# Kernel optimization log

Measured on AMD Instinct MI355X. Metric: run time of the kernel, lower is better.

Reference implementation:

```python
import jax, jax.numpy as jnp
import numpy as np

B, T, I, H = 512, 256, 64, 512
HN = 30  # hidden_nodes
EPS = 1e-5


def setup_inputs() -> dict:
    key = jax.random.key(0)
    ks = jax.random.split(key, 14)
    s = 0.05
    return {
        "x": jax.random.normal(ks[0], (B, T, I), jnp.float32),
        "W_ih": jax.random.normal(ks[1], (4 * H, I), jnp.float32) * s,
        "W_hh": jax.random.normal(ks[2], (4 * H, H), jnp.float32) * s,
        "b_ih": jax.random.normal(ks[3], (4 * H,), jnp.float32) * s,
        "b_hh": jax.random.normal(ks[4], (4 * H,), jnp.float32) * s,
        "l1_w": jax.random.normal(ks[5], (HN, H), jnp.float32) * s,
        "l1_b": jax.random.normal(ks[6], (HN,), jnp.float32) * s,
        "l2_w": jax.random.normal(ks[7], (HN, HN), jnp.float32) * s,
        "l3_w": jax.random.normal(ks[8], (HN, HN), jnp.float32) * s,
        "l4_w": jax.random.normal(ks[9], (HN, HN), jnp.float32) * s,
        "l5_w": jax.random.normal(ks[10], (2, HN), jnp.float32) * s,
        "bn_gamma": jnp.ones((HN,), jnp.float32),
        "bn_beta": jnp.zeros((HN,), jnp.float32),
    }


def _bn(a, gamma, beta):
    # training-mode BatchNorm1d: batch statistics over axis 0 (biased var)
    m = jnp.mean(a, axis=0)
    v = jnp.mean((a - m) ** 2, axis=0)
    return gamma * (a - m) * jax.lax.rsqrt(v + EPS) + beta


def reference(x, W_ih, W_hh, b_ih, b_hh, l1_w, l1_b, l2_w, l3_w, l4_w, l5_w,
              bn_gamma, bn_beta):
    def mlp(h):
        a = _bn(h @ l1_w.T + l1_b, bn_gamma, bn_beta)
        a = jax.nn.relu(a)
        a = jax.nn.relu(_bn(a @ l2_w.T, bn_gamma, bn_beta))
        a = jax.nn.relu(_bn(a @ l3_w.T, bn_gamma, bn_beta))
        a = jax.nn.relu(_bn(a @ l4_w.T, bn_gamma, bn_beta))
        return a @ l5_w.T  # [B, 2]

    def step(carry, x_t):
        h, c = carry
        gates = x_t @ W_ih.T + b_ih + h @ W_hh.T + b_hh  # [B, 4H]
        i_g, f_g, g_g, o_g = jnp.split(gates, 4, axis=1)  # torch order: i,f,g,o
        c = jax.nn.sigmoid(f_g) * c + jax.nn.sigmoid(i_g) * jnp.tanh(g_g)
        h = jax.nn.sigmoid(o_g) * jnp.tanh(c)
        return (h, c), mlp(h)

    h0 = jnp.zeros((x.shape[0], H), x.dtype)
    c0 = jnp.zeros((x.shape[0], H), x.dtype)
    xs = jnp.swapaxes(x, 0, 1)  # [T, B, I]
    _, outs = jax.lax.scan(step, (h0, c0), xs)  # [T, B, 2]
    return jnp.transpose(outs, (1, 2, 0))  # [B, 2, T]
```

## Files before the change

### kernel.cpp

```cpp
#include <hip/hip_runtime.h>
#include <math.h>

#define B_  512
#define T_  256
#define I_  64
#define H_  512
#define G4  2048
#define K_  576
#define HN  30
#define EPSf 1e-5f
#define GW  8
#define NG  32
#define BM  16
#define BJ  64
#define KP  520
#define A1P 32
#define HROT 4

typedef __attribute__((ext_vector_type(8))) short short8;
typedef __attribute__((ext_vector_type(4))) float f32x4;

static __device__ __forceinline__ unsigned short f2bf(float f) {
    unsigned int u = __float_as_uint(f);
    u += 0x7fffu + ((u >> 16) & 1u);
    return (unsigned short)(u >> 16);
}
static __device__ __forceinline__ float sigf(float x) {
    return __builtin_amdgcn_rcpf(1.0f + __expf(-x));
}
static __device__ __forceinline__ float tanh_f(float x) {
    float e = __expf(-2.0f * fabsf(x));
    float r = (1.0f - e) * __builtin_amdgcn_rcpf(1.0f + e);
    return copysignf(r, x);
}

__global__ void pack_kernel(const float* __restrict__ x, const float* __restrict__ Wih,
                            const float* __restrict__ Whh, const float* __restrict__ bih,
                            const float* __restrict__ bhh, const float* __restrict__ l1w,
                            unsigned short* __restrict__ Wp, unsigned short* __restrict__ xb,
                            float* __restrict__ bias, unsigned short* __restrict__ hb,
                            float* __restrict__ a1p, unsigned short* __restrict__ wl1b,
                            unsigned int* __restrict__ arr, unsigned int* __restrict__ map) {
    const int stride = gridDim.x * blockDim.x;
    const int g0 = blockIdx.x * blockDim.x + threadIdx.x;
    for (int idx = g0; idx < G4 * K_; idx += stride) {
        int n = idx / K_, k = idx - n * K_;
        float v = (k < H_) ? Whh[n * H_ + k] : Wih[n * I_ + (k - H_)];
        Wp[idx] = f2bf(v);
    }
    for (int idx = g0; idx < T_ * B_ * I_; idx += stride) {
        int t = idx / (B_ * I_);
        int r = idx - t * (B_ * I_);
        int b = r / I_, i = r - b * I_;
        xb[idx] = f2bf(x[((size_t)b * T_ + t) * I_ + i]);
    }
    for (int idx = g0; idx < G4; idx += stride) bias[idx] = bih[idx] + bhh[idx];
    for (int idx = g0; idx < B_ * H_; idx += stride) hb[idx] = 0;
    for (int idx = g0; idx < T_ * B_ * A1P; idx += stride) a1p[idx] = 0.0f;
    for (int idx = g0; idx < 32 * H_; idx += stride) {
        int f = idx >> 9, k = idx & 511;
        wl1b[idx] = (f < HN) ? f2bf(l1w[f * H_ + k]) : 0;
    }
    for (int idx = g0; idx < NG * 64; idx += stride) arr[idx] = 0u;
    for (int idx = g0; idx < 256; idx += stride) map[idx] = 0u;
}

__global__ __launch_bounds__(256, 1) void lstm_kernel(
        const unsigned short* __restrict__ Wp, const unsigned short* __restrict__ xb,
        const float* __restrict__ bias, unsigned short* __restrict__ hb,
        float* __restrict__ a1p, const unsigned short* __restrict__ wl1b,
        unsigned int* __restrict__ arr, unsigned int* __restrict__ map) {
    __shared__ unsigned short As[BM][KP];
    __shared__ unsigned short hsb[BM][72];
    __shared__ int flagLDS;

    const int tid  = threadIdx.x;
    const int w    = tid >> 6;
    const int lane = tid & 63;
    const int r    = lane & 15;
    const int q    = lane >> 4;
    const int mb   = blockIdx.x & 31;
    const int jb   = blockIdx.x >> 5;
    const int m0   = mb * BM;
    const int j0   = jb * BJ;
    const int hrow = tid >> 4, hseg = tid & 15;
    const int ft_l1 = w >> 1, kt_l1 = w & 1;

    if (tid == 0) {
        unsigned xcc;
        asm volatile("s_getreg_b32 %0, hwreg(HW_REG_XCC_ID)" : "=s"(xcc));
        __hip_atomic_store(&map[blockIdx.x], 0x100u | (xcc & 0xffu),
                           __ATOMIC_RELAXED, __HIP_MEMORY_SCOPE_AGENT);
    }

    short8 bfrag[4][18];
#pragma unroll
    for (int g = 0; g < 4; ++g)
#pragma unroll
        for (int kc = 0; kc < 18; ++kc) {
            bfrag[g][kc] = *reinterpret_cast<const short8*>(
                Wp + (size_t)(g * H_ + j0 + w * 16 + r) * K_ + kc * 32 + q * 8);
            asm volatile("" : "+v"(bfrag[g][kc]));
        }
    short8 bl1 = *reinterpret_cast<const short8*>(
        wl1b + (size_t)(ft_l1 * 16 + r) * H_ + j0 + kt_l1 * 32 + q * 8);
    asm volatile("" : "+v"(bl1));

    float bias_g[4];
#pragma unroll
    for (int g = 0; g < 4; ++g) bias_g[g] = bias[g * H_ + j0 + w * 16 + r];

    float c[4] = {0.f, 0.f, 0.f, 0.f};
    unsigned int* ctrA = arr + mb * 64;
    unsigned int* ctrB = arr + mb * 64 + 32;
    int fastf = 0;

#pragma unroll 1
    for (int t = 0; t < T_; ++t) {
        const unsigned short* hin = hb + (size_t)(t % HROT) * B_ * H_;
        unsigned short* hout      = hb + (size_t)((t + 1) % HROT) * B_ * H_;

        if (t > 0) {
            if (tid == 0) {
                if (fastf) {
                    const unsigned target = (unsigned)(GW * (t - 1));
                    unsigned tries = 0;
                    for (;;) {
                        unsigned old, zero = 0;
                        asm volatile("global_atomic_add %0, %1, %2, off sc0\n\t"
                                     "s_waitcnt vmcnt(0)"
                                     : "=&v"(old) : "v"(ctrB), "v"(zero) : "memory");
                        if (old >= target) break;
                        if (++tries > 100000u) break;
                        __builtin_amdgcn_s_sleep(1);
                    }
                } else {
                    const unsigned target = (unsigned)(GW * t);
                    unsigned tries = 0;
                    while (__hip_atomic_load(ctrA, __ATOMIC_RELAXED,
                                             __HIP_MEMORY_SCOPE_AGENT) < target) {
                        if (++tries > 100000u) break;
                        __builtin_amdgcn_s_sleep(1);
                    }
                    if (t == 1) {
                        unsigned v0 = __hip_atomic_load(&map[mb], __ATOMIC_RELAXED,
                                                        __HIP_MEMORY_SCOPE_AGENT);
                        int same = (v0 & 0x100u) ? 1 : 0;
                        for (int u = 1; u < GW; ++u) {
                            unsigned vu = __hip_atomic_load(&map[u * 32 + mb],
                                                            __ATOMIC_RELAXED,
                                                            __HIP_MEMORY_SCOPE_AGENT);
                            same &= (vu == v0);
                        }
                        flagLDS = same;
                    }
                }
            }
            __syncthreads();
            if (t == 1) fastf = flagLDS;
            asm volatile("" ::: "memory");
        }

        const unsigned short* xr = xb + ((size_t)t * B_ + m0 + r) * I_ + q * 8;
        const short8 xf0 = *reinterpret_cast<const short8*>(xr);
        const short8 xf1 = *reinterpret_cast<const short8*>(xr + 32);

        short8 hv[4];
        const unsigned short* hbase = hin + (size_t)(m0 + hrow) * H_ + hseg * 8;
        if (fastf) {
#pragma unroll
            for (int u = 0; u < 4; ++u)
                asm volatile("global_load_dwordx4 %0, %1, off sc0"
                             : "=&v"(hv[u]) : "v"(hbase + u * 128));
        } else {
#pragma unroll
            for (int u = 0; u < 4; ++u) {
                unsigned long long p2[2];
                p2[0] = __hip_atomic_load((const unsigned long long*)(hbase + u * 128),
                                          __ATOMIC_RELAXED, __HIP_MEMORY_SCOPE_AGENT);
                p2[1] = __hip_atomic_load((const unsigned long long*)(hbase + u * 128 + 4),
                                          __ATOMIC_RELAXED, __HIP_MEMORY_SCOPE_AGENT);
                __builtin_memcpy(&hv[u], p2, 16);
            }
        }
        asm volatile("s_waitcnt vmcnt(0)" ::: "memory");
        __builtin_amdgcn_sched_barrier(0);
#pragma unroll
        for (int u = 0; u < 4; ++u)
            *reinterpret_cast<short8*>(&As[hrow][u * 128 + hseg * 8]) = hv[u];
        __syncthreads();

        f32x4 acc[4];
#pragma unroll
        for (int g = 0; g < 4; ++g)
            acc[g] = (f32x4){bias_g[g], bias_g[g], bias_g[g], bias_g[g]};
#pragma unroll
        for (int kc = 0; kc < 16; ++kc) {
            const short8 afr = *reinterpret_cast<const short8*>(
                &As[r][kc * 32 + q * 8]);
#pragma unroll
            for (int g = 0; g < 4; ++g)
                acc[g] = __builtin_amdgcn_mfma_f32_16x16x32_bf16(
                    afr, bfrag[g][kc], acc[g], 0, 0, 0);
        }
#pragma unroll
        for (int g = 0; g < 4; ++g) {
            acc[g] = __builtin_amdgcn_mfma_f32_16x16x32_bf16(xf0, bfrag[g][16], acc[g], 0, 0, 0);
            acc[g] = __builtin_amdgcn_mfma_f32_16x16x32_bf16(xf1, bfrag[g][17], acc[g], 0, 0, 0);
        }

#pragma unroll
        for (int rr = 0; rr < 4; ++rr) {
            float ig = acc[0][rr], fg = acc[1][rr], gg = acc[2][rr], og = acc[3][rr];
            float cn = sigf(fg) * c[rr] + sigf(ig) * tanh_f(gg);
            c[rr] = cn;
            hsb[q * 4 + rr][w * 16 + r] = f2bf(sigf(og) * tanh_f(cn));
        }
        __syncthreads();

        {
            unsigned long long pv;
            __builtin_memcpy(&pv, &hsb[hrow][hseg * 4], 8);
            unsigned long long* hdst = (unsigned long long*)(hout
                + (size_t)(m0 + hrow) * H_ + j0 + hseg * 4);
            if (fastf) *hdst = pv;
            else __hip_atomic_store(hdst, pv, __ATOMIC_RELAXED,
                                    __HIP_MEMORY_SCOPE_AGENT);
        }

        if (t + 1 < T_) {
            asm volatile("s_waitcnt vmcnt(0)" ::: "memory");
            __syncthreads();
            if (tid == 0) {
                if (fastf) {
                    unsigned one = 1;
                    asm volatile("global_atomic_add %0, %1, off"
                                 :: "v"(ctrB), "v"(one) : "memory");
                } else {
                    __hip_atomic_fetch_add(ctrA, 1u, __ATOMIC_RELAXED,
                                           __HIP_MEMORY_SCOPE_AGENT);
                }
            }
        } else {
            __syncthreads();
        }

        const short8 ah = *reinterpret_cast<const short8*>(
            &hsb[r][kt_l1 * 32 + q * 8]);
        f32x4 d = __builtin_amdgcn_mfma_f32_16x16x32_bf16(
            ah, bl1, (f32x4){0.f, 0.f, 0.f, 0.f}, 0, 0, 0);
        const int f = ft_l1 * 16 + r;
        if (f < HN) {
            float* dst = a1p + ((size_t)t * B_ + m0 + q * 4) * A1P + f;
            if (fastf) {
#pragma unroll
                for (int rr = 0; rr < 4; ++rr) {
                    float* p = dst + rr * A1P;
                    asm volatile("global_atomic_add_f32 %0, %1, off"
                                 :: "v"(p), "v"(d[rr]) : "memory");
                }
            } else {
#pragma unroll
                for (int rr = 0; rr < 4; ++rr)
                    __hip_atomic_fetch_add(dst + rr * A1P, d[rr], __ATOMIC_RELAXED,
                                           __HIP_MEMORY_SCOPE_AGENT);
            }
        }
    }
}

static __device__ __forceinline__ void bn_relu30(float v[HN], const float* __restrict__ gamma,
                                                 const float* __restrict__ beta,
                                                 float (*pS)[HN], float (*pQ)[HN]) {
    float s0[HN], s1[HN];
#pragma unroll
    for (int f = 0; f < HN; ++f) { s0[f] = v[f]; s1[f] = v[f] * v[f]; }
#pragma unroll
    for (int off = 32; off >= 1; off >>= 1) {
#pragma unroll
        for (int f = 0; f < HN; ++f) {
            s0[f] += __shfl_xor(s0[f], off);
            s1[f] += __shfl_xor(s1[f], off);
        }
    }
    const int lane = threadIdx.x & 63, w = threadIdx.x >> 6;
    if (lane == 0) {
#pragma unroll
        for (int f = 0; f < HN; ++f) { pS[w][f] = s0[f]; pQ[w][f] = s1[f]; }
    }
    __syncthreads();
#pragma unroll
    for (int f = 0; f < HN; ++f) {
        float S = 0.f, Q = 0.f;
#pragma unroll
        for (int u = 0; u < 8; ++u) { S += pS[u][f]; Q += pQ[u][f]; }
        float m = S * (1.0f / 512.0f);
        float var = Q * (1.0f / 512.0f) - m * m;
        float inv = 1.0f / sqrtf(var + EPSf);
        float tv = gamma[f] * (v[f] - m) * inv + beta[f];
        v[f] = fmaxf(tv, 0.f);
    }
    __syncthreads();
}

static __device__ __forceinline__ void layer30(float v[HN], const float* __restrict__ w) {
    float u[HN];
#pragma unroll
    for (int f = 0; f < HN; ++f) {
        float a = 0.f;
#pragma unroll
        for (int k = 0; k < HN; ++k) a = fmaf(v[k], w[f * HN + k], a);
        u[f] = a;
    }
#pragma unroll
    for (int f = 0; f < HN; ++f) v[f] = u[f];
}

__global__ __launch_bounds__(512) void mlp_kernel(
        const float* __restrict__ a1p, const float* __restrict__ l1b,
        const float* __restrict__ l2w, const float* __restrict__ l3w,
        const float* __restrict__ l4w, const float* __restrict__ l5w,
        const float* __restrict__ gamma, const float* __restrict__ beta,
        float* __restrict__ out) {
    const int t = blockIdx.x;
    const int b = threadIdx.x;
    __shared__ float pS[8][HN], pQ[8][HN];
    float v[HN];
    const float* src = a1p + ((size_t)t * B_ + b) * A1P;
#pragma unroll
    for (int f = 0; f < HN; ++f) v[f] = src[f] + l1b[f];
    bn_relu30(v, gamma, beta, pS, pQ);
    layer30(v, l2w); bn_relu30(v, gamma, beta, pS, pQ);
    layer30(v, l3w); bn_relu30(v, gamma, beta, pS, pQ);
    layer30(v, l4w); bn_relu30(v, gamma, beta, pS, pQ);
    float o0 = 0.f, o1 = 0.f;
#pragma unroll
    for (int k = 0; k < HN; ++k) {
        o0 = fmaf(v[k], l5w[k], o0);
        o1 = fmaf(v[k], l5w[HN + k], o1);
    }
    out[(size_t)b * (2 * T_) + t]      = o0;
    out[(size_t)b * (2 * T_) + T_ + t] = o1;
}

extern "C" void kernel_launch(void* const* d_in, const int* in_sizes, int n_in,
                              void* d_out, int out_size, void* d_ws, size_t ws_size,
                              hipStream_t stream) {
    const float* x    = (const float*)d_in[0];
    const float* Wih  = (const float*)d_in[1];
    const float* Whh  = (const float*)d_in[2];
    const float* bih  = (const float*)d_in[3];
    const float* bhh  = (const float*)d_in[4];
    const float* l1w  = (const float*)d_in[5];
    const float* l1b  = (const float*)d_in[6];
    const float* l2w  = (const float*)d_in[7];
    const float* l3w  = (const float*)d_in[8];
    const float* l4w  = (const float*)d_in[9];
    const float* l5w  = (const float*)d_in[10];
    const float* gam  = (const float*)d_in[11];
    const float* bet  = (const float*)d_in[12];
    float* out = (float*)d_out;

    char* ws = (char*)d_ws;
    unsigned short* Wp   = (unsigned short*)ws;  ws += (size_t)G4 * K_ * 2;
    unsigned short* xb   = (unsigned short*)ws;  ws += (size_t)T_ * B_ * I_ * 2;
    float*          bia  = (float*)ws;           ws += (size_t)G4 * 4;
    unsigned short* hb   = (unsigned short*)ws;  ws += (size_t)HROT * B_ * H_ * 2;
    float*          a1p  = (float*)ws;           ws += (size_t)T_ * B_ * A1P * 4;
    unsigned short* wl1b = (unsigned short*)ws;  ws += (size_t)32 * H_ * 2;
    unsigned int*   arr  = (unsigned int*)ws;    ws += (size_t)NG * 64 * 4;
    unsigned int*   map  = (unsigned int*)ws;    ws += (size_t)256 * 4;

    pack_kernel<<<1024, 256, 0, stream>>>(x, Wih, Whh, bih, bhh, l1w,
                                          Wp, xb, bia, hb, a1p, wl1b, arr, map);
    lstm_kernel<<<NG * GW, 256, 0, stream>>>(Wp, xb, bia, hb, a1p, wl1b, arr, map);
    mlp_kernel<<<T_, 512, 0, stream>>>(a1p, l1b, l2w, l3w, l4w, l5w, gam, bet, out);
}
```

Measured before the change: 907.8 us.

## Read fp32 x directly in LSTM kernel and store h without LDS staging sync

Removes the pre-pass that transposed and converted x to bf16. The LSTM kernel now loads fp32 x rows for each step before the barrier wait and converts them in registers. The h output is written straight to global memory from each lane as 2-byte stores, dropping one __syncthreads and the LDS round trip. This saves a large pack pass and hides the x load latency, but the per-lane scattered 16-bit global stores may coalesce worse than the old 8-byte stores.

```diff
diff --git a/kernel.cpp b/kernel.cpp
--- a/kernel.cpp
+++ b/kernel.cpp
@@ -34,12 +34,12 @@
     return copysignf(r, x);
 }
 
-__global__ void pack_kernel(const float* __restrict__ x, const float* __restrict__ Wih,
-                            const float* __restrict__ Whh, const float* __restrict__ bih,
-                            const float* __restrict__ bhh, const float* __restrict__ l1w,
-                            unsigned short* __restrict__ Wp, unsigned short* __restrict__ xb,
-                            float* __restrict__ bias, unsigned short* __restrict__ hb,
-                            float* __restrict__ a1p, unsigned short* __restrict__ wl1b,
+__global__ void pack_kernel(const float* __restrict__ Wih, const float* __restrict__ Whh,
+                            const float* __restrict__ bih, const float* __restrict__ bhh,
+                            const float* __restrict__ l1w,
+                            unsigned short* __restrict__ Wp, float* __restrict__ bias,
+                            unsigned short* __restrict__ hb, float* __restrict__ a1p,
+                            unsigned short* __restrict__ wl1b,
                             unsigned int* __restrict__ arr, unsigned int* __restrict__ map) {
     const int stride = gridDim.x * blockDim.x;
     const int g0 = blockIdx.x * blockDim.x + threadIdx.x;
@@ -48,12 +48,6 @@
         float v = (k < H_) ? Whh[n * H_ + k] : Wih[n * I_ + (k - H_)];
         Wp[idx] = f2bf(v);
     }
-    for (int idx = g0; idx < T_ * B_ * I_; idx += stride) {
-        int t = idx / (B_ * I_);
-        int r = idx - t * (B_ * I_);
-        int b = r / I_, i = r - b * I_;
-        xb[idx] = f2bf(x[((size_t)b * T_ + t) * I_ + i]);
-    }
     for (int idx = g0; idx < G4; idx += stride) bias[idx] = bih[idx] + bhh[idx];
     for (int idx = g0; idx < B_ * H_; idx += stride) hb[idx] = 0;
     for (int idx = g0; idx < T_ * B_ * A1P; idx += stride) a1p[idx] = 0.0f;
@@ -66,7 +60,7 @@
 }
 
 __global__ __launch_bounds__(256, 1) void lstm_kernel(
-        const unsigned short* __restrict__ Wp, const unsigned short* __restrict__ xb,
+        const unsigned short* __restrict__ Wp, const float* __restrict__ x,
         const float* __restrict__ bias, unsigned short* __restrict__ hb,
         float* __restrict__ a1p, const unsigned short* __restrict__ wl1b,
         unsigned int* __restrict__ arr, unsigned int* __restrict__ map) {
@@ -119,6 +113,12 @@
     for (int t = 0; t < T_; ++t) {
         const unsigned short* hin = hb + (size_t)(t % HROT) * B_ * H_;
         unsigned short* hout      = hb + (size_t)((t + 1) % HROT) * B_ * H_;
+
+        const float* xrow = x + ((size_t)(m0 + r) * T_ + t) * I_ + q * 8;
+        const f32x4 fa = *reinterpret_cast<const f32x4*>(xrow);
+        const f32x4 fb = *reinterpret_cast<const f32x4*>(xrow + 4);
+        const f32x4 fc = *reinterpret_cast<const f32x4*>(xrow + 32);
+        const f32x4 fd = *reinterpret_cast<const f32x4*>(xrow + 36);
 
         if (t > 0) {
             if (tid == 0) {
@@ -161,10 +161,6 @@
             asm volatile("" ::: "memory");
         }
 
-        const unsigned short* xr = xb + ((size_t)t * B_ + m0 + r) * I_ + q * 8;
-        const short8 xf0 = *reinterpret_cast<const short8*>(xr);
-        const short8 xf1 = *reinterpret_cast<const short8*>(xr + 32);
-
         short8 hv[4];
         const unsigned short* hbase = hin + (size_t)(m0 + hrow) * H_ + hseg * 8;
         if (fastf) {
@@ -190,6 +186,15 @@
             *reinterpret_cast<short8*>(&As[hrow][u * 128 + hseg * 8]) = hv[u];
         __syncthreads();
 
+        short8 xf0, xf1;
+#pragma unroll
+        for (int e = 0; e < 4; ++e) {
+            xf0[e]     = (short)f2bf(fa[e]);
+            xf0[e + 4] = (short)f2bf(fb[e]);
+            xf1[e]     = (short)f2bf(fc[e]);
+            xf1[e + 4] = (short)f2bf(fd[e]);
+        }
+
         f32x4 acc[4];
 #pragma unroll
         for (int g = 0; g < 4; ++g)
@@ -214,17 +219,12 @@
             float ig = acc[0][rr], fg = acc[1][rr], gg = acc[2][rr], og = acc[3][rr];
             float cn = sigf(fg) * c[rr] + sigf(ig) * tanh_f(gg);
             c[rr] = cn;
-            hsb[q * 4 + rr][w * 16 + r] = f2bf(sigf(og) * tanh_f(cn));
-        }
-        __syncthreads();
-
-        {
-            unsigned long long pv;
-            __builtin_memcpy(&pv, &hsb[hrow][hseg * 4], 8);
-            unsigned long long* hdst = (unsigned long long*)(hout
-                + (size_t)(m0 + hrow) * H_ + j0 + hseg * 4);
-            if (fastf) *hdst = pv;
-            else __hip_atomic_store(hdst, pv, __ATOMIC_RELAXED,
+            unsigned short hvs = f2bf(sigf(og) * tanh_f(cn));
+            hsb[q * 4 + rr][w * 16 + r] = hvs;
+            unsigned short* hdst = hout + (size_t)(m0 + q * 4 + rr) * H_
+                                   + j0 + w * 16 + r;
+            if (fastf) *hdst = hvs;
+            else __hip_atomic_store(hdst, hvs, __ATOMIC_RELAXED,
                                     __HIP_MEMORY_SCOPE_AGENT);
         }
 
@@ -363,7 +363,6 @@
 
     char* ws = (char*)d_ws;
     unsigned short* Wp   = (unsigned short*)ws;  ws += (size_t)G4 * K_ * 2;
-    unsigned short* xb   = (unsigned short*)ws;  ws += (size_t)T_ * B_ * I_ * 2;
     float*          bia  = (float*)ws;           ws += (size_t)G4 * 4;
     unsigned short* hb   = (unsigned short*)ws;  ws += (size_t)HROT * B_ * H_ * 2;
     float*          a1p  = (float*)ws;           ws += (size_t)T_ * B_ * A1P * 4;
@@ -371,8 +370,8 @@
     unsigned int*   arr  = (unsigned int*)ws;    ws += (size_t)NG * 64 * 4;
     unsigned int*   map  = (unsigned int*)ws;    ws += (size_t)256 * 4;
 
-    pack_kernel<<<1024, 256, 0, stream>>>(x, Wih, Whh, bih, bhh, l1w,
-                                          Wp, xb, bia, hb, a1p, wl1b, arr, map);
-    lstm_kernel<<<NG * GW, 256, 0, stream>>>(Wp, xb, bia, hb, a1p, wl1b, arr, map);
+    pack_kernel<<<1024, 256, 0, stream>>>(Wih, Whh, bih, bhh, l1w,
+                                          Wp, bia, hb, a1p, wl1b, arr, map);
+    lstm_kernel<<<NG * GW, 256, 0, stream>>>(Wp, x, bia, hb, a1p, wl1b, arr, map);
     mlp_kernel<<<T_, 512, 0, stream>>>(a1p, l1b, l2w, l3w, l4w, l5w, gam, bet, out);
 }
```

Result: slower. 945.1 us (+4.1%).
